# Kernel tuning notes

Measured on AMD Instinct MI355X. Metric: run time of the kernel, lower is better.

## Reference

```python
import jax, jax.numpy as jnp
import numpy as np

N_PAPER, N_MESH = 60000, 30000
N = N_PAPER + N_MESH
E_TRAIN, E_DEC = 2000000, 400000
F_PAPER = F_MESH = 128
D0, H, D = 16, 32, 16  # initial embed, hidden, final embed
NREL, NB = 2, 4


def _glorot(key, shape):
    fan_in, fan_out = shape[-2], shape[-1]
    s = jnp.sqrt(6.0 / (fan_in + fan_out)).astype(jnp.float32)
    return jax.random.uniform(key, shape, jnp.float32, -s, s)


def setup_inputs() -> dict:
    key = jax.random.key(0)
    ks = iter(jax.random.split(key, 40))
    inp = {
        'x_paper': jax.random.normal(next(ks), (N_PAPER, F_PAPER), jnp.float32),
        'x_mesh': jax.random.normal(next(ks), (N_MESH, F_MESH), jnp.float32),
        'train_edge_index': jax.random.randint(next(ks), (2, E_TRAIN), 0, N, jnp.int64 if jax.config.jax_enable_x64 else jnp.int32),
        'train_edge_type': jnp.sort(jax.random.randint(next(ks), (E_TRAIN,), 0, NREL)),
        'pos_edge_index': jax.random.randint(next(ks), (2, E_DEC), 0, N),
        'pos_edge_type': jnp.sort(jax.random.randint(next(ks), (E_DEC,), 0, NREL)),
        'neg_edge_index': jax.random.randint(next(ks), (2, E_DEC), 0, N),
        'neg_edge_type': jnp.sort(jax.random.randint(next(ks), (E_DEC,), 0, NREL)),
        # input transforms
        'Wp': _glorot(next(ks), (F_PAPER, D0)), 'bp': jnp.zeros((D0,), jnp.float32),
        'Wm': _glorot(next(ks), (F_MESH, D0)), 'bm': jnp.zeros((D0,), jnp.float32),
        # decode linears
        'Wd0': _glorot(next(ks), (D, D)), 'bd0': jnp.zeros((D,), jnp.float32),
        'Wd1': _glorot(next(ks), (D, D)), 'bd1': jnp.zeros((D,), jnp.float32),
    }
    dims = [(D0, H), (H, H), (H, H), (H, D)]
    for i, (di, do) in enumerate(dims, 1):
        inp[f'bases{i}'] = _glorot(next(ks), (NB, di, do))
        inp[f'comp{i}'] = _glorot(next(ks), (NREL, NB))
        inp[f'root{i}'] = _glorot(next(ks), (di, do))
        inp[f'bias{i}'] = jnp.zeros((do,), jnp.float32)
    return inp


def rgcn_layer(x, src, dst, et, bases, comp, root, bias):
    # PyG RGCNConv with basis decomposition, per-relation mean aggregation.
    out = x @ root + bias
    xs = x[src]  # [E, in]
    for r in range(NREL):
        W_r = jnp.einsum('b,bio->io', comp[r], bases)
        m = xs @ W_r  # [E, out]
        mf = (et == r).astype(m.dtype)
        cnt = jax.ops.segment_sum(mf, dst, num_segments=N)
        agg = jax.ops.segment_sum(m * mf[:, None], dst, num_segments=N)
        out = out + agg / jnp.clip(cnt, 1.0)[:, None]
    return out


def _decode_block(z, ei, et, Wd0, bd0, Wd1, bd1):
    zs, zd = z[ei[0]], z[ei[1]]
    h0 = zs @ Wd0 + bd0
    h1 = zs @ Wd1 + bd1
    h = jnp.where((et == 0)[:, None], h0, h1)
    return jnp.sum(h * zd, axis=-1)


def reference(x_paper, x_mesh, train_edge_index, train_edge_type,
              pos_edge_index, pos_edge_type, neg_edge_index, neg_edge_type,
              Wp, bp, Wm, bm, Wd0, bd0, Wd1, bd1,
              bases1, comp1, root1, bias1, bases2, comp2, root2, bias2,
              bases3, comp3, root3, bias3, bases4, comp4, root4, bias4):
    x = jnp.concatenate([x_paper @ Wp + bp, x_mesh @ Wm + bm], axis=0)  # [N, D0]
    src, dst = train_edge_index[0], train_edge_index[1]
    x = jax.nn.relu(rgcn_layer(x, src, dst, train_edge_type, bases1, comp1, root1, bias1))
    x = jax.nn.relu(rgcn_layer(x, src, dst, train_edge_type, bases2, comp2, root2, bias2))
    x = jax.nn.relu(rgcn_layer(x, src, dst, train_edge_type, bases3, comp3, root3, bias3))
    z = rgcn_layer(x, src, dst, train_edge_type, bases4, comp4, root4, bias4)
    # edge types are sorted, so per-edge in-order compute matches the masked concat order
    pos = _decode_block(z, pos_edge_index, pos_edge_type, Wd0, bd0, Wd1, bd1)
    neg = _decode_block(z, neg_edge_index, neg_edge_type, Wd0, bd0, Wd1, bd1)
    return jnp.concatenate([pos, neg], axis=0)  # [2*E_DEC]
```

## Files before the change

### kernel.cpp

```cpp
#include <hip/hip_runtime.h>
#include <hip/hip_bf16.h>

constexpr int NN = 90000;
constexpr int NP = 60000;
constexpr int NM = 30000;
constexpr int ET = 2000000;
constexpr int ED = 400000;
constexpr int TWO_NN = 2 * NN;

constexpr int BKT_SH  = 9;
constexpr int NB_BKT  = (TWO_NN + 511) >> BKT_SH;
constexpr int BKT_CAP = 6400;
constexpr int TILE    = 2048;
constexpr int N_TILES = (ET + TILE - 1) / TILE;
constexpr int NG = 8;

__device__ __forceinline__ float bflo(unsigned int u) {
    union { unsigned int i; float f; } c;
    c.i = u << 16;
    return c.f;
}
__device__ __forceinline__ float bfhi(unsigned int u) {
    union { unsigned int i; float f; } c;
    c.i = u & 0xffff0000u;
    return c.f;
}
__device__ __forceinline__ unsigned short f2bf(float f) {
    union { float f; unsigned int i; } c;
    c.f = f;
    unsigned int x = c.i;
    return (unsigned short)((x + 0x7FFFu + ((x >> 16) & 1u)) >> 16);
}

__global__ void init_kernel(const int* __restrict__ tei, int* __restrict__ gcur,
                            int* __restrict__ dflag) {
    int b = blockIdx.x * blockDim.x + threadIdx.x;
    if (b < NB_BKT) gcur[b] = b * BKT_CAP;
    if (b == 0) {
        int allzero = 1;
        for (int i = 0; i < 16; i++)
            if (tei[2 * i + 1] != 0) allzero = 0;
        dflag[0] = allzero;
    }
}

__global__ void __launch_bounds__(256) binA_kernel(
        const int* __restrict__ ei, const int* __restrict__ et,
        const int* __restrict__ dflag, int* __restrict__ gcur,
        int2* __restrict__ pairs) {
    __shared__ int histw[4][NB_BKT];
    __shared__ int wbase[4][NB_BKT];
    __shared__ int tot[NB_BKT];
    __shared__ int excl[NB_BKT];
    __shared__ int gbase[NB_BKT];
    __shared__ int scn[256];
    __shared__ int2 tbuf[TILE];
    int t = threadIdx.x;
    int w = t >> 6;
    int tile0 = blockIdx.x * TILE;
    int tcount = ET - tile0;
    if (tcount > TILE) tcount = TILE;
    for (int i = t; i < 4 * NB_BKT; i += 256) ((int*)histw)[i] = 0;
    __syncthreads();
    int sft = dflag[0];
    int myk[8], mys[8];
#pragma unroll
    for (int q = 0; q < 8; q++) {
        int li = q * 256 + t;
        myk[q] = -1;
        if (li < tcount) {
            int e = tile0 + li;
            int s = ei[(size_t)e << sft];
            int d = ei[(size_t)(ET + e) << sft];
            int r = et[(size_t)e << sft];
            int key = r * NN + d;
            myk[q] = key;
            mys[q] = s;
            atomicAdd(&histw[w][key >> BKT_SH], 1);
        }
    }
    __syncthreads();
    for (int i = t; i < NB_BKT; i += 256) {
        int h0 = histw[0][i], h1 = histw[1][i], h2 = histw[2][i], h3 = histw[3][i];
        wbase[0][i] = 0;
        wbase[1][i] = h0;
        wbase[2][i] = h0 + h1;
        wbase[3][i] = h0 + h1 + h2;
        tot[i] = h0 + h1 + h2 + h3;
    }
    __syncthreads();
    int v0 = (t < NB_BKT / 2) ? tot[2 * t] : 0;
    int v1 = (t < NB_BKT / 2) ? tot[2 * t + 1] : 0;
    int s = v0 + v1;
    scn[t] = s;
    __syncthreads();
    for (int st = 1; st < 256; st <<= 1) {
        int u = (t >= st) ? scn[t - st] : 0;
        __syncthreads();
        scn[t] += u;
        __syncthreads();
    }
    int base = scn[t] - s;
    if (t < NB_BKT / 2) {
        excl[2 * t] = base;
        excl[2 * t + 1] = base + v0;
    }
    __syncthreads();
    for (int i = t; i < NB_BKT; i += 256) {
        int e0 = excl[i];
        wbase[0][i] += e0;
        wbase[1][i] += e0;
        wbase[2][i] += e0;
        wbase[3][i] += e0;
        histw[0][i] = 0; histw[1][i] = 0; histw[2][i] = 0; histw[3][i] = 0;
    }
    __syncthreads();
#pragma unroll
    for (int q = 0; q < 8; q++) {
        if (myk[q] >= 0) {
            int b = myk[q] >> BKT_SH;
            int p = wbase[w][b] + atomicAdd(&histw[w][b], 1);
            tbuf[p] = make_int2(myk[q], mys[q]);
        }
    }
    __syncthreads();
    for (int i = t; i < NB_BKT; i += 256)
        if (tot[i] > 0) gbase[i] = atomicAdd(&gcur[i], tot[i]);
    __syncthreads();
    for (int i = t; i < tcount; i += 256) {
        int2 p = tbuf[i];
        int b = p.x >> BKT_SH;
        int gpos = gbase[b] + (i - excl[b]);
        int cap = (b + 1) * BKT_CAP - 1;
        pairs[gpos < cap ? gpos : cap] = p;
    }
}

__global__ void __launch_bounds__(256) histplace_kernel(
        const int* __restrict__ gcur, const int2* __restrict__ pairs,
        int* __restrict__ off, int* __restrict__ endo, float* __restrict__ inv,
        int* __restrict__ csr) {
    __shared__ int kh[512 * NG];
    __shared__ int scn[256];
    int b = blockIdx.x;
    int t = threadIdx.x;
    int beg = b * BKT_CAP, end = gcur[b];
    for (int i = t; i < 512 * NG; i += 256) kh[i] = 0;
    __syncthreads();
    for (int i = beg + t; i < end; i += 256) {
        int2 p = pairs[i];
        atomicAdd(&kh[(p.x & 511) * NG + (p.y >> 14)], 1);
    }
    __syncthreads();
    int cnt[2][NG];
    int v[2];
    int s = 0;
#pragma unroll
    for (int q = 0; q < 2; q++) {
        int key = t * 2 + q;
        v[q] = 0;
#pragma unroll
        for (int g = 0; g < NG; g++) {
            cnt[q][g] = kh[key * NG + g];
            v[q] += cnt[q][g];
        }
        s += v[q];
    }
    scn[t] = s;
    __syncthreads();
    for (int st = 1; st < 256; st <<= 1) {
        int u = (t >= st) ? scn[t - st] : 0;
        __syncthreads();
        scn[t] += u;
        __syncthreads();
    }
    int run = beg + scn[t] - s;
    int kbase = b << BKT_SH;
#pragma unroll
    for (int q = 0; q < 2; q++) {
        int key = kbase + t * 2 + q;
        if (key < TWO_NN) {
            off[key] = run;
            endo[key] = run + v[q];
            inv[key] = 1.0f / (float)(v[q] > 1 ? v[q] : 1);
        }
        int gb = run;
#pragma unroll
        for (int g = 0; g < NG; g++) {
            kh[(t * 2 + q) * NG + g] = gb;
            gb += cnt[q][g];
        }
        run += v[q];
    }
    __syncthreads();
    for (int i = beg + t; i < end; i += 256) {
        int2 p = pairs[i];
        int pos = atomicAdd(&kh[(p.x & 511) * NG + (p.y >> 14)], 1);
        csr[pos] = p.y;
    }
}

__global__ void __launch_bounds__(256) embed2_kernel(
        const float* __restrict__ Xp, const float* __restrict__ Xm,
        const float* __restrict__ Wp, const float* __restrict__ bp,
        const float* __restrict__ Wm, const float* __restrict__ bm,
        unsigned short* __restrict__ outbf) {
    __shared__ float Wl[4096 + 32];
    for (int i = threadIdx.x; i < 2048; i += 256) {
        Wl[i] = Wp[i];
        Wl[2048 + i] = Wm[i];
    }
    if (threadIdx.x < 16) {
        Wl[4096 + threadIdx.x] = bp[threadIdx.x];
        Wl[4112 + threadIdx.x] = bm[threadIdx.x];
    }
    __syncthreads();
    int n = blockIdx.x * 256 + threadIdx.x;
    if (n >= NN) return;
    const float* X;
    const float* Ws;
    const float* Bs;
    if (n < NP) { X = Xp + (size_t)n * 128; Ws = Wl; Bs = Wl + 4096; }
    else        { X = Xm + (size_t)(n - NP) * 128; Ws = Wl + 2048; Bs = Wl + 4112; }
    float acc[16];
#pragma unroll
    for (int j = 0; j < 16; j++) acc[j] = Bs[j];
    const float4* row = (const float4*)X;
    for (int k4 = 0; k4 < 32; k4++) {
        float4 xv = row[k4];
        int k = k4 * 4;
#pragma unroll
        for (int j = 0; j < 16; j++) {
            float a = acc[j];
            a = fmaf(xv.x, Ws[(k + 0) * 16 + j], a);
            a = fmaf(xv.y, Ws[(k + 1) * 16 + j], a);
            a = fmaf(xv.z, Ws[(k + 2) * 16 + j], a);
            a = fmaf(xv.w, Ws[(k + 3) * 16 + j], a);
            acc[j] = a;
        }
    }
    ushort4* ob = (ushort4*)(outbf + (size_t)n * 16);
#pragma unroll
    for (int q = 0; q < 4; q++) {
        ushort4 ub;
        ub.x = f2bf(acc[4 * q]);     ub.y = f2bf(acc[4 * q + 1]);
        ub.z = f2bf(acc[4 * q + 2]); ub.w = f2bf(acc[4 * q + 3]);
        ob[q] = ub;
    }
}

__global__ void prep_all_kernel(
        const float* __restrict__ ba0, const float* __restrict__ co0,
        const float* __restrict__ ro0, const float* __restrict__ bi0,
        const float* __restrict__ ba1, const float* __restrict__ co1,
        const float* __restrict__ ro1, const float* __restrict__ bi1,
        const float* __restrict__ ba2, const float* __restrict__ co2,
        const float* __restrict__ ro2, const float* __restrict__ bi2,
        const float* __restrict__ ba3, const float* __restrict__ co3,
        const float* __restrict__ ro3, const float* __restrict__ bi3,
        float* __restrict__ Wbuf4) {
    int l = blockIdx.x;
    const float* bases; const float* comp; const float* root; const float* bias;
    if (l == 0)      { bases = ba0; comp = co0; root = ro0; bias = bi0; }
    else if (l == 1) { bases = ba1; comp = co1; root = ro1; bias = bi1; }
    else if (l == 2) { bases = ba2; comp = co2; root = ro2; bias = bi2; }
    else             { bases = ba3; comp = co3; root = ro3; bias = bi3; }
    int din = (l == 0) ? 16 : 32;
    int dout = (l == 3) ? 16 : 32;
    int sz = din * dout;
    float* W = Wbuf4 + l * 3200;
    for (int i = threadIdx.x; i < sz; i += 256) {
        float b0 = bases[i];
        float b1 = bases[sz + i];
        float b2 = bases[2 * sz + i];
        float b3 = bases[3 * sz + i];
        for (int r = 0; r < 2; r++) {
            W[r * sz + i] = comp[r * 4 + 0] * b0 + comp[r * 4 + 1] * b1 +
                            comp[r * 4 + 2] * b2 + comp[r * 4 + 3] * b3;
        }
        W[2 * sz + i] = root[i];
    }
    if (threadIdx.x < dout) W[3 * sz + threadIdx.x] = bias[threadIdx.x];
}

template <int DIN, int DOUT, int RELU>
__global__ void __launch_bounds__(256) layer_kernel(
        const int* __restrict__ off, const int* __restrict__ endo,
        const int* __restrict__ csr,
        const unsigned short* __restrict__ xbf_in,
        const float* __restrict__ inv, const float* __restrict__ Wbuf,
        unsigned short* __restrict__ xbf_out) {
    constexpr int SZ = DIN * DOUT;
    constexpr int QL = DIN / 8;
    constexpr int TPN = 2 * QL;
    constexpr int NPB = 256 / TPN;
    constexpr int AGST = 2 * DIN + 4;
    constexpr int XSST = DIN + 8;
    __shared__ float Wl[3 * SZ + DOUT];
    __shared__ float agg[NPB * AGST];
    __shared__ unsigned short xsu[NPB * XSST];
    for (int i = threadIdx.x; i < 3 * SZ + DOUT; i += 256) Wl[i] = Wbuf[i];
    int t = threadIdx.x;
    int ln = t / TPN;
    int rl = t % TPN;
    int r = rl / QL;
    int lane = rl % QL;
    int d = blockIdx.x * NPB + ln;
    if (d < NN) {
        if (r == 0) {
            uint4 u = *(const uint4*)(xbf_in + (size_t)d * DIN + lane * 8);
            *(uint4*)&xsu[ln * XSST + lane * 8] = u;
        }
        int key = r * NN + d;
        int b = off[key];
        int e = endo[key];
        float a0[8] = {0, 0, 0, 0, 0, 0, 0, 0};
        float a1[8] = {0, 0, 0, 0, 0, 0, 0, 0};
        const unsigned short* hp = xbf_in + lane * 8;
        int k = b;
        if (k + 3 < e) {
            int s0 = csr[k], s1 = csr[k + 1], s2 = csr[k + 2], s3 = csr[k + 3];
            k += 4;
            while (k + 3 < e) {
                uint4 u0 = *(const uint4*)(hp + (size_t)s0 * DIN);
                uint4 u1 = *(const uint4*)(hp + (size_t)s1 * DIN);
                uint4 u2 = *(const uint4*)(hp + (size_t)s2 * DIN);
                uint4 u3 = *(const uint4*)(hp + (size_t)s3 * DIN);
                s0 = csr[k]; s1 = csr[k + 1]; s2 = csr[k + 2]; s3 = csr[k + 3];
                k += 4;
                a0[0] += bflo(u0.x); a0[1] += bfhi(u0.x);
                a0[2] += bflo(u0.y); a0[3] += bfhi(u0.y);
                a0[4] += bflo(u0.z); a0[5] += bfhi(u0.z);
                a0[6] += bflo(u0.w); a0[7] += bfhi(u0.w);
                a1[0] += bflo(u1.x); a1[1] += bfhi(u1.x);
                a1[2] += bflo(u1.y); a1[3] += bfhi(u1.y);
                a1[4] += bflo(u1.z); a1[5] += bfhi(u1.z);
                a1[6] += bflo(u1.w); a1[7] += bfhi(u1.w);
                a0[0] += bflo(u2.x); a0[1] += bfhi(u2.x);
                a0[2] += bflo(u2.y); a0[3] += bfhi(u2.y);
                a0[4] += bflo(u2.z); a0[5] += bfhi(u2.z);
                a0[6] += bflo(u2.w); a0[7] += bfhi(u2.w);
                a1[0] += bflo(u3.x); a1[1] += bfhi(u3.x);
                a1[2] += bflo(u3.y); a1[3] += bfhi(u3.y);
                a1[4] += bflo(u3.z); a1[5] += bfhi(u3.z);
                a1[6] += bflo(u3.w); a1[7] += bfhi(u3.w);
            }
            uint4 u0 = *(const uint4*)(hp + (size_t)s0 * DIN);
            uint4 u1 = *(const uint4*)(hp + (size_t)s1 * DIN);
            uint4 u2 = *(const uint4*)(hp + (size_t)s2 * DIN);
            uint4 u3 = *(const uint4*)(hp + (size_t)s3 * DIN);
            a0[0] += bflo(u0.x); a0[1] += bfhi(u0.x);
            a0[2] += bflo(u0.y); a0[3] += bfhi(u0.y);
            a0[4] += bflo(u0.z); a0[5] += bfhi(u0.z);
            a0[6] += bflo(u0.w); a0[7] += bfhi(u0.w);
            a1[0] += bflo(u1.x); a1[1] += bfhi(u1.x);
            a1[2] += bflo(u1.y); a1[3] += bfhi(u1.y);
            a1[4] += bflo(u1.z); a1[5] += bfhi(u1.z);
            a1[6] += bflo(u1.w); a1[7] += bfhi(u1.w);
            a0[0] += bflo(u2.x); a0[1] += bfhi(u2.x);
            a0[2] += bflo(u2.y); a0[3] += bfhi(u2.y);
            a0[4] += bflo(u2.z); a0[5] += bfhi(u2.z);
            a0[6] += bflo(u2.w); a0[7] += bfhi(u2.w);
            a1[0] += bflo(u3.x); a1[1] += bfhi(u3.x);
            a1[2] += bflo(u3.y); a1[3] += bfhi(u3.y);
            a1[4] += bflo(u3.z); a1[5] += bfhi(u3.z);
            a1[6] += bflo(u3.w); a1[7] += bfhi(u3.w);
        }
        for (; k < e; k++) {
            uint4 u0 = *(const uint4*)(hp + (size_t)csr[k] * DIN);
            a0[0] += bflo(u0.x); a0[1] += bfhi(u0.x);
            a0[2] += bflo(u0.y); a0[3] += bfhi(u0.y);
            a0[4] += bflo(u0.z); a0[5] += bfhi(u0.z);
            a0[6] += bflo(u0.w); a0[7] += bfhi(u0.w);
        }
        float* ap = agg + ln * AGST + r * DIN + lane * 8;
        *(float4*)ap = make_float4(a0[0] + a1[0], a0[1] + a1[1],
                                   a0[2] + a1[2], a0[3] + a1[3]);
        *(float4*)(ap + 4) = make_float4(a0[4] + a1[4], a0[5] + a1[5],
                                         a0[6] + a1[6], a0[7] + a1[7]);
    }
    __syncthreads();
    constexpr int CPN = DOUT / 4;
    for (int tt = t; tt < NPB * CPN; tt += 256) {
        int ln2 = tt / CPN;
        int j0 = (tt % CPN) * 4;
        int d2 = blockIdx.x * NPB + ln2;
        if (d2 < NN) {
            float iv0 = inv[d2], iv1 = inv[NN + d2];
            float acc[4];
#pragma unroll
            for (int jj = 0; jj < 4; jj++) acc[jj] = Wl[3 * SZ + j0 + jj];
#pragma unroll
            for (int k2 = 0; k2 < DIN; k2 += 2) {
                unsigned up = *(const unsigned*)&xsu[ln2 * XSST + k2];
                float xv0 = bflo(up);
                float xv1 = bfhi(up);
                float m00 = agg[ln2 * AGST + k2] * iv0;
                float m10 = agg[ln2 * AGST + DIN + k2] * iv1;
                float m01 = agg[ln2 * AGST + k2 + 1] * iv0;
                float m11 = agg[ln2 * AGST + DIN + k2 + 1] * iv1;
                const float* w0a = &Wl[k2 * DOUT + j0];
                const float* w1a = &Wl[SZ + k2 * DOUT + j0];
                const float* wra = &Wl[2 * SZ + k2 * DOUT + j0];
#pragma unroll
                for (int jj = 0; jj < 4; jj++) {
                    acc[jj] = fmaf(xv0, wra[jj], acc[jj]);
                    acc[jj] = fmaf(m00, w0a[jj], acc[jj]);
                    acc[jj] = fmaf(m10, w1a[jj], acc[jj]);
                    acc[jj] = fmaf(xv1, wra[DOUT + jj], acc[jj]);
                    acc[jj] = fmaf(m01, w0a[DOUT + jj], acc[jj]);
                    acc[jj] = fmaf(m11, w1a[DOUT + jj], acc[jj]);
                }
            }
            if (RELU) {
#pragma unroll
                for (int jj = 0; jj < 4; jj++) acc[jj] = fmaxf(acc[jj], 0.0f);
            }
            ushort4 ub;
            ub.x = f2bf(acc[0]); ub.y = f2bf(acc[1]);
            ub.z = f2bf(acc[2]); ub.w = f2bf(acc[3]);
            *(ushort4*)(xbf_out + (size_t)d2 * DOUT + j0) = ub;
        }
    }
}

__global__ void __launch_bounds__(256) decode_fused_kernel(
        const unsigned short* __restrict__ zbf,
        const float* __restrict__ Wd0, const float* __restrict__ bd0,
        const float* __restrict__ Wd1, const float* __restrict__ bd1,
        const int* __restrict__ pei, const int* __restrict__ pet,
        const int* __restrict__ nei, const int* __restrict__ net_,
        float* __restrict__ out, const int* __restrict__ dflag) {
    __shared__ float W[2][256];
    __shared__ float B[2][16];
    for (int i = threadIdx.x; i < 256; i += 256) {
        W[0][i] = Wd0[i];
        W[1][i] = Wd1[i];
    }
    if (threadIdx.x < 16) {
        B[0][threadIdx.x] = bd0[threadIdx.x];
        B[1][threadIdx.x] = bd1[threadIdx.x];
    }
    __syncthreads();
    int i = blockIdx.x * 256 + threadIdx.x;
    if (i >= 2 * ED) return;
    int sft = dflag[0];
    const int* ei;
    const int* et;
    int e;
    if (i < ED) { ei = pei; et = pet; e = i; }
    else        { ei = nei; et = net_; e = i - ED; }
    int s = ei[(size_t)e << sft];
    int d = ei[(size_t)(ED + e) << sft];
    int r = et[(size_t)e << sft];
    float zs[16], zd[16];
    const uint4* sp = (const uint4*)(zbf + ((size_t)s << 4));
    const uint4* dp = (const uint4*)(zbf + ((size_t)d << 4));
#pragma unroll
    for (int h = 0; h < 2; h++) {
        uint4 us = sp[h];
        uint4 ud = dp[h];
        int o8 = h * 8;
        zs[o8 + 0] = bflo(us.x); zs[o8 + 1] = bfhi(us.x);
        zs[o8 + 2] = bflo(us.y); zs[o8 + 3] = bfhi(us.y);
        zs[o8 + 4] = bflo(us.z); zs[o8 + 5] = bfhi(us.z);
        zs[o8 + 6] = bflo(us.w); zs[o8 + 7] = bfhi(us.w);
        zd[o8 + 0] = bflo(ud.x); zd[o8 + 1] = bfhi(ud.x);
        zd[o8 + 2] = bflo(ud.y); zd[o8 + 3] = bfhi(ud.y);
        zd[o8 + 4] = bflo(ud.z); zd[o8 + 5] = bfhi(ud.z);
        zd[o8 + 6] = bflo(ud.w); zd[o8 + 7] = bfhi(ud.w);
    }
    const float* Wr = W[r];
    const float* Br = B[r];
    float acc = 0.0f;
#pragma unroll
    for (int j = 0; j < 16; j++) {
        float yj = Br[j];
#pragma unroll
        for (int k = 0; k < 16; k++) yj = fmaf(zs[k], Wr[k * 16 + j], yj);
        acc = fmaf(yj, zd[j], acc);
    }
    out[i] = acc;
}

extern "C" void kernel_launch(void* const* d_in, const int* in_sizes, int n_in,
                              void* d_out, int out_size, void* d_ws, size_t ws_size,
                              hipStream_t stream) {
    const float* x_paper = (const float*)d_in[0];
    const float* x_mesh  = (const float*)d_in[1];
    const int* tei  = (const int*)d_in[2];
    const int* tet  = (const int*)d_in[3];
    const int* pei  = (const int*)d_in[4];
    const int* pet  = (const int*)d_in[5];
    const int* nei  = (const int*)d_in[6];
    const int* net_ = (const int*)d_in[7];
    const float* Wp  = (const float*)d_in[8];
    const float* bp  = (const float*)d_in[9];
    const float* Wm  = (const float*)d_in[10];
    const float* bm  = (const float*)d_in[11];
    const float* Wd0 = (const float*)d_in[12];
    const float* bd0 = (const float*)d_in[13];
    const float* Wd1 = (const float*)d_in[14];
    const float* bd1 = (const float*)d_in[15];

    float* ws = (float*)d_ws;
    size_t o = 0;
    unsigned short* xbfA = (unsigned short*)(ws + o); o += (size_t)NN * 16;
    unsigned short* xbfB = (unsigned short*)(ws + o); o += (size_t)NN * 16;
    float* inv  = ws + o; o += (size_t)TWO_NN;
    int*   off  = (int*)(ws + o); o += (size_t)TWO_NN;
    int*   endo = (int*)(ws + o); o += (size_t)TWO_NN;
    int*   csr  = (int*)(ws + o); o += (size_t)NB_BKT * BKT_CAP;
    int*   gcur = (int*)(ws + o); o += 512;
    int2*  pairs = (int2*)(ws + o); o += (size_t)2 * NB_BKT * BKT_CAP;
    float* Wbuf4 = ws + o; o += 4 * 3200;
    int*   dflag = (int*)(ws + o); o += 16;

    init_kernel<<<(NB_BKT + 255) / 256, 256, 0, stream>>>(tei, gcur, dflag);

    binA_kernel<<<N_TILES, 256, 0, stream>>>(tei, tet, dflag, gcur, pairs);
    histplace_kernel<<<NB_BKT, 256, 0, stream>>>(gcur, pairs, off, endo, inv, csr);

    embed2_kernel<<<(NN + 255) / 256, 256, 0, stream>>>(
        x_paper, x_mesh, Wp, bp, Wm, bm, xbfA);

    prep_all_kernel<<<4, 256, 0, stream>>>(
        (const float*)d_in[16], (const float*)d_in[17], (const float*)d_in[18], (const float*)d_in[19],
        (const float*)d_in[20], (const float*)d_in[21], (const float*)d_in[22], (const float*)d_in[23],
        (const float*)d_in[24], (const float*)d_in[25], (const float*)d_in[26], (const float*)d_in[27],
        (const float*)d_in[28], (const float*)d_in[29], (const float*)d_in[30], (const float*)d_in[31],
        Wbuf4);

    int blk16 = (NN + 63) / 64;
    int blk32 = (NN + 31) / 32;
    layer_kernel<16, 32, 1><<<blk16, 256, 0, stream>>>(
        off, endo, csr, xbfA, inv, Wbuf4 + 0 * 3200, xbfB);
    layer_kernel<32, 32, 1><<<blk32, 256, 0, stream>>>(
        off, endo, csr, xbfB, inv, Wbuf4 + 1 * 3200, xbfA);
    layer_kernel<32, 32, 1><<<blk32, 256, 0, stream>>>(
        off, endo, csr, xbfA, inv, Wbuf4 + 2 * 3200, xbfB);
    layer_kernel<32, 16, 0><<<blk32, 256, 0, stream>>>(
        off, endo, csr, xbfB, inv, Wbuf4 + 3 * 3200, xbfA);

    decode_fused_kernel<<<(2 * ED + 255) / 256, 256, 0, stream>>>(
        xbfA, Wd0, bd0, Wd1, bd1, pei, pet, nei, net_, (float*)d_out, dflag);
}
```

Baseline: 353.2 us.

## Sort destination nodes by degree to balance per-warp gather work in layers

Builds a degree histogram, scans it, and scatters node ids into a degree-sorted permutation, which the four layer kernels then use to pick which destination node each thread group handles. Grouping nodes of similar in-degree in the same wavefront is meant to reduce divergence and tail imbalance in the gather loops. It adds three small kernels, an atomic-ordered permutation, and loses the contiguous access pattern for self-features and output writes.

```diff
diff --git a/kernel.cpp b/kernel.cpp
--- a/kernel.cpp
+++ b/kernel.cpp
@@ -33,9 +33,10 @@
 }
 
 __global__ void init_kernel(const int* __restrict__ tei, int* __restrict__ gcur,
-                            int* __restrict__ dflag) {
+                            int* __restrict__ dflag, int* __restrict__ dhist) {
     int b = blockIdx.x * blockDim.x + threadIdx.x;
     if (b < NB_BKT) gcur[b] = b * BKT_CAP;
+    if (b < 256) dhist[b] = 0;
     if (b == 0) {
         int allzero = 1;
         for (int i = 0; i < 16; i++)
@@ -197,6 +198,48 @@
         int2 p = pairs[i];
         int pos = atomicAdd(&kh[(p.x & 511) * NG + (p.y >> 14)], 1);
         csr[pos] = p.y;
+    }
+}
+
+__global__ void deghist_kernel(const int* __restrict__ off,
+                               const int* __restrict__ endo,
+                               int* __restrict__ dhist) {
+    int d = blockIdx.x * 256 + threadIdx.x;
+    if (d < NN) {
+        int d0 = endo[d] - off[d];
+        int d1 = endo[NN + d] - off[NN + d];
+        int m = d0 > d1 ? d0 : d1;
+        if (m > 255) m = 255;
+        atomicAdd(&dhist[m], 1);
+    }
+}
+__global__ void degscan_kernel(const int* __restrict__ dhist,
+                               int* __restrict__ dcur) {
+    __shared__ int s[256];
+    int t = threadIdx.x;
+    int v = dhist[t];
+    s[t] = v;
+    __syncthreads();
+    for (int st = 1; st < 256; st <<= 1) {
+        int u = (t >= st) ? s[t - st] : 0;
+        __syncthreads();
+        s[t] += u;
+        __syncthreads();
+    }
+    dcur[t] = s[t] - v;
+}
+__global__ void permscat_kernel(const int* __restrict__ off,
+                                const int* __restrict__ endo,
+                                int* __restrict__ dcur,
+                                int* __restrict__ perm) {
+    int d = blockIdx.x * 256 + threadIdx.x;
+    if (d < NN) {
+        int d0 = endo[d] - off[d];
+        int d1 = endo[NN + d] - off[NN + d];
+        int m = d0 > d1 ? d0 : d1;
+        if (m > 255) m = 255;
+        int pos = atomicAdd(&dcur[m], 1);
+        perm[pos] = d;
     }
 }
 
@@ -286,7 +329,7 @@
 template <int DIN, int DOUT, int RELU>
 __global__ void __launch_bounds__(256) layer_kernel(
         const int* __restrict__ off, const int* __restrict__ endo,
-        const int* __restrict__ csr,
+        const int* __restrict__ csr, const int* __restrict__ perm,
         const unsigned short* __restrict__ xbf_in,
         const float* __restrict__ inv, const float* __restrict__ Wbuf,
         unsigned short* __restrict__ xbf_out) {
@@ -299,14 +342,17 @@
     __shared__ float Wl[3 * SZ + DOUT];
     __shared__ float agg[NPB * AGST];
     __shared__ unsigned short xsu[NPB * XSST];
+    __shared__ int dmap[NPB];
     for (int i = threadIdx.x; i < 3 * SZ + DOUT; i += 256) Wl[i] = Wbuf[i];
     int t = threadIdx.x;
     int ln = t / TPN;
     int rl = t % TPN;
     int r = rl / QL;
     int lane = rl % QL;
-    int d = blockIdx.x * NPB + ln;
-    if (d < NN) {
+    int slot = blockIdx.x * NPB + ln;
+    if (slot < NN) {
+        int d = perm[slot];
+        if (rl == 0) dmap[ln] = d;
         if (r == 0) {
             uint4 u = *(const uint4*)(xbf_in + (size_t)d * DIN + lane * 8);
             *(uint4*)&xsu[ln * XSST + lane * 8] = u;
@@ -384,8 +430,9 @@
     for (int tt = t; tt < NPB * CPN; tt += 256) {
         int ln2 = tt / CPN;
         int j0 = (tt % CPN) * 4;
-        int d2 = blockIdx.x * NPB + ln2;
-        if (d2 < NN) {
+        int slot2 = blockIdx.x * NPB + ln2;
+        if (slot2 < NN) {
+            int d2 = dmap[ln2];
             float iv0 = inv[d2], iv1 = inv[NN + d2];
             float acc[4];
 #pragma unroll
@@ -515,11 +562,19 @@
     int2*  pairs = (int2*)(ws + o); o += (size_t)2 * NB_BKT * BKT_CAP;
     float* Wbuf4 = ws + o; o += 4 * 3200;
     int*   dflag = (int*)(ws + o); o += 16;
-
-    init_kernel<<<(NB_BKT + 255) / 256, 256, 0, stream>>>(tei, gcur, dflag);
+    int*   perm  = (int*)(ws + o); o += (size_t)NN;
+    int*   dhist = (int*)(ws + o); o += 256;
+    int*   dcur  = (int*)(ws + o); o += 256;
+
+    init_kernel<<<(NB_BKT + 255) / 256, 256, 0, stream>>>(tei, gcur, dflag, dhist);
 
     binA_kernel<<<N_TILES, 256, 0, stream>>>(tei, tet, dflag, gcur, pairs);
     histplace_kernel<<<NB_BKT, 256, 0, stream>>>(gcur, pairs, off, endo, inv, csr);
+
+    int blkn = (NN + 255) / 256;
+    deghist_kernel<<<blkn, 256, 0, stream>>>(off, endo, dhist);
+    degscan_kernel<<<1, 256, 0, stream>>>(dhist, dcur);
+    permscat_kernel<<<blkn, 256, 0, stream>>>(off, endo, dcur, perm);
 
     embed2_kernel<<<(NN + 255) / 256, 256, 0, stream>>>(
         x_paper, x_mesh, Wp, bp, Wm, bm, xbfA);
@@ -534,13 +589,13 @@
     int blk16 = (NN + 63) / 64;
     int blk32 = (NN + 31) / 32;
     layer_kernel<16, 32, 1><<<blk16, 256, 0, stream>>>(
-        off, endo, csr, xbfA, inv, Wbuf4 + 0 * 3200, xbfB);
+        off, endo, csr, perm, xbfA, inv, Wbuf4 + 0 * 3200, xbfB);
     layer_kernel<32, 32, 1><<<blk32, 256, 0, stream>>>(
-        off, endo, csr, xbfB, inv, Wbuf4 + 1 * 3200, xbfA);
+        off, endo, csr, perm, xbfB, inv, Wbuf4 + 1 * 3200, xbfA);
     layer_kernel<32, 32, 1><<<blk32, 256, 0, stream>>>(
-        off, endo, csr, xbfA, inv, Wbuf4 + 2 * 3200, xbfB);
+        off, endo, csr, perm, xbfA, inv, Wbuf4 + 2 * 3200, xbfB);
     layer_kernel<32, 16, 0><<<blk32, 256, 0, stream>>>(
-        off, endo, csr, xbfB, inv, Wbuf4 + 3 * 3200, xbfA);
+        off, endo, csr, perm, xbfB, inv, Wbuf4 + 3 * 3200, xbfA);
 
     decode_fused_kernel<<<(2 * ED + 255) / 256, 256, 0, stream>>>(
         xbfA, Wd0, bd0, Wd1, bd1, pei, pet, nei, net_, (float*)d_out, dflag);
```

Result: slower. 1.004 ms (+184.2%).
